# Kernel tuning notes

Hardware: AMD Instinct MI355X
Metric: run time of the kernel (lower is better)

The kernel has to match this reference:

```python
import jax, jax.numpy as jnp
import numpy as np

MARGIN = 0.0625  # init kwarg `margin`; barrier = relu


def setup_inputs() -> dict:
    key = jax.random.key(0)
    k1, k2, k3, k4 = jax.random.split(key, 4)
    B, N, M = 64, 64, 100000
    return {
        "outputs": jax.random.normal(k1, (B, N, 3), dtype=jnp.float32),
        "c2ws": jax.random.normal(k2, (B, 4, 4), dtype=jnp.float32),
        "scene_scales": jax.random.uniform(k3, (B,), dtype=jnp.float32),
        "means": jax.random.normal(k4, (M, 3), dtype=jnp.float32),
    }


def reference(outputs, c2ws, scene_scales, means):
    # aff = R * s (per-batch scaled rotation block), trans = translation column
    aff = c2ws[:, :3, :3] * scene_scales[:, None, None]      # [B,3,3]
    trans = c2ws[:, :3, 3]                                   # [B,3]
    # retrajs = baddbmm(trans, outputs, aff.mT) = outputs @ aff^T + trans
    retrajs = jnp.einsum("bnj,bij->bni", outputs, aff) + trans[:, None, :]
    q = retrajs.reshape(-1, 3)                               # [Q,3], Q = B*N
    # Brute-force nearest neighbor (replaces kd_tree.query); torch_kdtree
    # returns SQUARED euclidean distances, so we keep d^2.
    # d2[q,m] = |q|^2 + |m|^2 - 2 q.m  -> [Q,M] (the dominant memory-bound op)
    d2 = (
        jnp.sum(q * q, axis=-1, keepdims=True)
        + jnp.sum(means * means, axis=-1)[None, :]
        - 2.0 * (q @ means.T)
    )
    dists = jnp.maximum(jnp.min(d2, axis=1), 0.0)            # [Q]
    loss = jnp.mean(jax.nn.relu(-(dists - MARGIN)))
    return loss
```

## Files before the change

### kernel.cpp

```cpp
#include <hip/hip_runtime.h>
#include <hip/hip_bf16.h>

#define MARGIN 0.0625f

#define P 4096
#define M 100000
#define G 500
#define CHUNK 200
#define NPAIR (CHUNK / 2)
#define QS 2
#define R 8
#define HSEG 16

typedef float float2v __attribute__((ext_vector_type(2)));

#define WS_XS_OFF      0
#define WS_YS_OFF      400000
#define WS_ZS_OFF      800000
#define WS_MS_OFF      1200000
#define WS_PARTIAL_OFF 1600000
#define WS_PART2_OFF   9792000

__global__ __launch_bounds__(256) void prep_kernel(
    const float* __restrict__ means,
    float* __restrict__ xs, float* __restrict__ ys,
    float* __restrict__ zs, float* __restrict__ ms,
    float* __restrict__ out)
{
    int idx = blockIdx.x * 256 + threadIdx.x;
    if (idx == 0) out[0] = 0.0f;
    if (idx < M) {
        float x = means[3 * idx + 0];
        float y = means[3 * idx + 1];
        float z = means[3 * idx + 2];
        xs[idx] = -2.0f * x;
        ys[idx] = -2.0f * y;
        zs[idx] = -2.0f * z;
        ms[idx] = fmaf(x, x, fmaf(y, y, z * z));
    }
}

__global__ __launch_bounds__(256, 4) void nn_kernel(
    const float* __restrict__ outputs,
    const float* __restrict__ c2ws,
    const float* __restrict__ scales,
    const float* __restrict__ xs, const float* __restrict__ ys,
    const float* __restrict__ zs, const float* __restrict__ ms,
    float* __restrict__ partial)
{
    const int t  = threadIdx.x;
    const int g  = blockIdx.x;
    const int qs = blockIdx.y;
    const int pbase = qs * (P / QS);
    const int mbase = g * CHUNK;

    __shared__ float2v lxs[NPAIR], lys[NPAIR], lzs[NPAIR], lms[NPAIR];

    if (t < NPAIR) {
        lxs[t] = *(const float2v*)(xs + mbase + 2 * t);
        lys[t] = *(const float2v*)(ys + mbase + 2 * t);
        lzs[t] = *(const float2v*)(zs + mbase + 2 * t);
        lms[t] = *(const float2v*)(ms + mbase + 2 * t);
    }

    float2v qxs[R], qys[R], qzs[R], mn[R];
    float qq[R];
#pragma unroll
    for (int i = 0; i < R; ++i) {
        int p = pbase + i * 256 + t;
        int b = p >> 6;
        float s  = scales[b];
        float o0 = outputs[3 * p + 0];
        float o1 = outputs[3 * p + 1];
        float o2 = outputs[3 * p + 2];
        const float* cw = c2ws + b * 16;
        float q0 = fmaf(s, fmaf(cw[0],  o0, fmaf(cw[1],  o1, cw[2]  * o2)), cw[3]);
        float q1 = fmaf(s, fmaf(cw[4],  o0, fmaf(cw[5],  o1, cw[6]  * o2)), cw[7]);
        float q2 = fmaf(s, fmaf(cw[8],  o0, fmaf(cw[9],  o1, cw[10] * o2)), cw[11]);
        qq[i] = fmaf(q0, q0, fmaf(q1, q1, q2 * q2));
        qxs[i] = (float2v){q0, q0};
        qys[i] = (float2v){q1, q1};
        qzs[i] = (float2v){q2, q2};
        mn[i]  = (float2v){1e30f, 1e30f};
    }

    __syncthreads();

#pragma unroll 4
    for (int j = 0; j < NPAIR; ++j) {
        float2v cx = lxs[j];
        float2v cy = lys[j];
        float2v cz = lzs[j];
        float2v cm = lms[j];
#pragma unroll
        for (int i = 0; i < R; ++i) {
            float2v d = __builtin_elementwise_fma(qzs[i], cz,
                        __builtin_elementwise_fma(qys[i], cy,
                        __builtin_elementwise_fma(qxs[i], cx, cm)));
            mn[i] = __builtin_elementwise_min(mn[i], d);
        }
    }

#pragma unroll
    for (int i = 0; i < R; ++i) {
        int p = pbase + i * 256 + t;
        float m = fminf(mn[i][0], mn[i][1]);
        partial[g * P + p] = fmaxf(qq[i] + m, 0.0f);
    }
}

__global__ __launch_bounds__(256) void reduce1_kernel(
    const float* __restrict__ partial,
    float* __restrict__ partial2)
{
    const int t = threadIdx.x;
    const int s = blockIdx.x;
    const int h = blockIdx.y;
    const int q = s * 256 + t;

    const int gbeg = h * 32;
    const int gend = (gbeg + 32 < G) ? gbeg + 32 : G;

    float m = 1e30f;
#pragma unroll 4
    for (int g = gbeg; g < gend; ++g)
        m = fminf(m, partial[g * P + q]);

    partial2[h * P + q] = m;
}

__global__ __launch_bounds__(256) void reduce2_kernel(
    const float* __restrict__ partial2,
    float* __restrict__ out)
{
    const int t = threadIdx.x;
    const int q = blockIdx.x * 256 + t;

    float m = 1e30f;
#pragma unroll
    for (int h = 0; h < HSEG; ++h)
        m = fminf(m, partial2[h * P + q]);

    float v = fmaxf(MARGIN - m, 0.0f) * (1.0f / (float)P);

#pragma unroll
    for (int off = 32; off > 0; off >>= 1)
        v += __shfl_down(v, off, 64);

    __shared__ float lds[4];
    int wid = t >> 6;
    if ((t & 63) == 0) lds[wid] = v;
    __syncthreads();
    if (t == 0)
        atomicAdd(out, lds[0] + lds[1] + lds[2] + lds[3]);
}

extern "C" void kernel_launch(void* const* d_in, const int* in_sizes, int n_in,
                              void* d_out, int out_size, void* d_ws, size_t ws_size,
                              hipStream_t stream) {
    const float* outputs = (const float*)d_in[0];
    const float* c2ws    = (const float*)d_in[1];
    const float* scales  = (const float*)d_in[2];
    const float* means   = (const float*)d_in[3];

    char* ws = (char*)d_ws;
    float* xs       = (float*)(ws + WS_XS_OFF);
    float* ys       = (float*)(ws + WS_YS_OFF);
    float* zs       = (float*)(ws + WS_ZS_OFF);
    float* ms       = (float*)(ws + WS_MS_OFF);
    float* partial  = (float*)(ws + WS_PARTIAL_OFF);
    float* partial2 = (float*)(ws + WS_PART2_OFF);
    float* out      = (float*)d_out;

    prep_kernel<<<(M + 255) / 256, 256, 0, stream>>>(means, xs, ys, zs, ms, out);
    nn_kernel<<<dim3(G, QS), 256, 0, stream>>>(outputs, c2ws, scales,
                                               xs, ys, zs, ms, partial);
    reduce1_kernel<<<dim3(16, HSEG), 256, 0, stream>>>(partial, partial2);
    reduce2_kernel<<<16, 256, 0, stream>>>(partial2, out);
}
```

Measured before the change: 104.4 us.

## Fuse means prep and partial-min reduction into NN kernel via atomicMin

Removes the separate prep kernel by having each block read raw means, scale them by -2 and compute their squared norms straight into shared memory. The partial-min buffer and two reduction kernels are replaced by a per-query atomicMin on float bits, seeded by a memset to 0xFF, plus a small finish kernel. The inner loop now reads float4 LDS values and splits them into two float2 halves. This removes large global round-trips and launches, at the cost of global atomic contention (500 blocks per query) and strided 3-float means loads in every block.

```diff
diff --git a/kernel.cpp b/kernel.cpp
--- a/kernel.cpp
+++ b/kernel.cpp
@@ -1,5 +1,4 @@
 #include <hip/hip_runtime.h>
-#include <hip/hip_bf16.h>
 
 #define MARGIN 0.0625f
 
@@ -7,46 +6,21 @@
 #define M 100000
 #define G 500
 #define CHUNK 200
-#define NPAIR (CHUNK / 2)
+#define NQUAD (CHUNK / 4)
 #define QS 2
 #define R 8
-#define HSEG 16
 
 typedef float float2v __attribute__((ext_vector_type(2)));
+typedef float float4v __attribute__((ext_vector_type(4)));
 
-#define WS_XS_OFF      0
-#define WS_YS_OFF      400000
-#define WS_ZS_OFF      800000
-#define WS_MS_OFF      1200000
-#define WS_PARTIAL_OFF 1600000
-#define WS_PART2_OFF   9792000
-
-__global__ __launch_bounds__(256) void prep_kernel(
-    const float* __restrict__ means,
-    float* __restrict__ xs, float* __restrict__ ys,
-    float* __restrict__ zs, float* __restrict__ ms,
-    float* __restrict__ out)
-{
-    int idx = blockIdx.x * 256 + threadIdx.x;
-    if (idx == 0) out[0] = 0.0f;
-    if (idx < M) {
-        float x = means[3 * idx + 0];
-        float y = means[3 * idx + 1];
-        float z = means[3 * idx + 2];
-        xs[idx] = -2.0f * x;
-        ys[idx] = -2.0f * y;
-        zs[idx] = -2.0f * z;
-        ms[idx] = fmaf(x, x, fmaf(y, y, z * z));
-    }
-}
+#define WS_PMIN_OFF 0
 
 __global__ __launch_bounds__(256, 4) void nn_kernel(
     const float* __restrict__ outputs,
     const float* __restrict__ c2ws,
     const float* __restrict__ scales,
-    const float* __restrict__ xs, const float* __restrict__ ys,
-    const float* __restrict__ zs, const float* __restrict__ ms,
-    float* __restrict__ partial)
+    const float* __restrict__ means,
+    unsigned int* __restrict__ pmin)
 {
     const int t  = threadIdx.x;
     const int g  = blockIdx.x;
@@ -54,13 +28,15 @@
     const int pbase = qs * (P / QS);
     const int mbase = g * CHUNK;
 
-    __shared__ float2v lxs[NPAIR], lys[NPAIR], lzs[NPAIR], lms[NPAIR];
+    __shared__ float4v lxs[NQUAD], lys[NQUAD], lzs[NQUAD], lms[NQUAD];
 
-    if (t < NPAIR) {
-        lxs[t] = *(const float2v*)(xs + mbase + 2 * t);
-        lys[t] = *(const float2v*)(ys + mbase + 2 * t);
-        lzs[t] = *(const float2v*)(zs + mbase + 2 * t);
-        lms[t] = *(const float2v*)(ms + mbase + 2 * t);
+    if (t < CHUNK) {
+        const float* mp = means + 3 * (mbase + t);
+        float x = mp[0], y = mp[1], z = mp[2];
+        ((float*)lxs)[t] = -2.0f * x;
+        ((float*)lys)[t] = -2.0f * y;
+        ((float*)lzs)[t] = -2.0f * z;
+        ((float*)lms)[t] = fmaf(x, x, fmaf(y, y, z * z));
     }
 
     float2v qxs[R], qys[R], qzs[R], mn[R];
@@ -77,7 +53,7 @@
         float q0 = fmaf(s, fmaf(cw[0],  o0, fmaf(cw[1],  o1, cw[2]  * o2)), cw[3]);
         float q1 = fmaf(s, fmaf(cw[4],  o0, fmaf(cw[5],  o1, cw[6]  * o2)), cw[7]);
         float q2 = fmaf(s, fmaf(cw[8],  o0, fmaf(cw[9],  o1, cw[10] * o2)), cw[11]);
-        qq[i] = fmaf(q0, q0, fmaf(q1, q1, q2 * q2));
+        qq[i]  = fmaf(q0, q0, fmaf(q1, q1, q2 * q2));
         qxs[i] = (float2v){q0, q0};
         qys[i] = (float2v){q1, q1};
         qzs[i] = (float2v){q2, q2};
@@ -86,18 +62,30 @@
 
     __syncthreads();
 
-#pragma unroll 4
-    for (int j = 0; j < NPAIR; ++j) {
-        float2v cx = lxs[j];
-        float2v cy = lys[j];
-        float2v cz = lzs[j];
-        float2v cm = lms[j];
+#pragma unroll 2
+    for (int j = 0; j < NQUAD; ++j) {
+        float4v cx4 = lxs[j];
+        float4v cy4 = lys[j];
+        float4v cz4 = lzs[j];
+        float4v cm4 = lms[j];
+        float2v cx0 = __builtin_shufflevector(cx4, cx4, 0, 1);
+        float2v cx1 = __builtin_shufflevector(cx4, cx4, 2, 3);
+        float2v cy0 = __builtin_shufflevector(cy4, cy4, 0, 1);
+        float2v cy1 = __builtin_shufflevector(cy4, cy4, 2, 3);
+        float2v cz0 = __builtin_shufflevector(cz4, cz4, 0, 1);
+        float2v cz1 = __builtin_shufflevector(cz4, cz4, 2, 3);
+        float2v cm0 = __builtin_shufflevector(cm4, cm4, 0, 1);
+        float2v cm1 = __builtin_shufflevector(cm4, cm4, 2, 3);
 #pragma unroll
         for (int i = 0; i < R; ++i) {
-            float2v d = __builtin_elementwise_fma(qzs[i], cz,
-                        __builtin_elementwise_fma(qys[i], cy,
-                        __builtin_elementwise_fma(qxs[i], cx, cm)));
-            mn[i] = __builtin_elementwise_min(mn[i], d);
+            float2v d0 = __builtin_elementwise_fma(qzs[i], cz0,
+                         __builtin_elementwise_fma(qys[i], cy0,
+                         __builtin_elementwise_fma(qxs[i], cx0, cm0)));
+            float2v d1 = __builtin_elementwise_fma(qzs[i], cz1,
+                         __builtin_elementwise_fma(qys[i], cy1,
+                         __builtin_elementwise_fma(qxs[i], cx1, cm1)));
+            mn[i] = __builtin_elementwise_min(mn[i], d0);
+            mn[i] = __builtin_elementwise_min(mn[i], d1);
         }
     }
 
@@ -105,42 +93,20 @@
     for (int i = 0; i < R; ++i) {
         int p = pbase + i * 256 + t;
         float m = fminf(mn[i][0], mn[i][1]);
-        partial[g * P + p] = fmaxf(qq[i] + m, 0.0f);
+        float d = fmaxf(qq[i] + m, 0.0f);
+        unsigned int bits = __float_as_uint(d);
+        if (bits < pmin[p]) atomicMin(&pmin[p], bits);
     }
 }
 
-__global__ __launch_bounds__(256) void reduce1_kernel(
-    const float* __restrict__ partial,
-    float* __restrict__ partial2)
-{
-    const int t = threadIdx.x;
-    const int s = blockIdx.x;
-    const int h = blockIdx.y;
-    const int q = s * 256 + t;
-
-    const int gbeg = h * 32;
-    const int gend = (gbeg + 32 < G) ? gbeg + 32 : G;
-
-    float m = 1e30f;
-#pragma unroll 4
-    for (int g = gbeg; g < gend; ++g)
-        m = fminf(m, partial[g * P + q]);
-
-    partial2[h * P + q] = m;
-}
-
-__global__ __launch_bounds__(256) void reduce2_kernel(
-    const float* __restrict__ partial2,
+__global__ __launch_bounds__(256) void finish_kernel(
+    const unsigned int* __restrict__ pmin,
     float* __restrict__ out)
 {
     const int t = threadIdx.x;
     const int q = blockIdx.x * 256 + t;
 
-    float m = 1e30f;
-#pragma unroll
-    for (int h = 0; h < HSEG; ++h)
-        m = fminf(m, partial2[h * P + q]);
-
+    float m = __uint_as_float(pmin[q]);
     float v = fmaxf(MARGIN - m, 0.0f) * (1.0f / (float)P);
 
 #pragma unroll
@@ -163,18 +129,12 @@
     const float* scales  = (const float*)d_in[2];
     const float* means   = (const float*)d_in[3];
 
-    char* ws = (char*)d_ws;
-    float* xs       = (float*)(ws + WS_XS_OFF);
-    float* ys       = (float*)(ws + WS_YS_OFF);
-    float* zs       = (float*)(ws + WS_ZS_OFF);
-    float* ms       = (float*)(ws + WS_MS_OFF);
-    float* partial  = (float*)(ws + WS_PARTIAL_OFF);
-    float* partial2 = (float*)(ws + WS_PART2_OFF);
-    float* out      = (float*)d_out;
+    unsigned int* pmin = (unsigned int*)((char*)d_ws + WS_PMIN_OFF);
+    float* out = (float*)d_out;
 
-    prep_kernel<<<(M + 255) / 256, 256, 0, stream>>>(means, xs, ys, zs, ms, out);
-    nn_kernel<<<dim3(G, QS), 256, 0, stream>>>(outputs, c2ws, scales,
-                                               xs, ys, zs, ms, partial);
-    reduce1_kernel<<<dim3(16, HSEG), 256, 0, stream>>>(partial, partial2);
-    reduce2_kernel<<<16, 256, 0, stream>>>(partial2, out);
+    hipMemsetAsync(pmin, 0xFF, P * sizeof(unsigned int), stream);
+    hipMemsetAsync(out, 0, sizeof(float), stream);
+
+    nn_kernel<<<dim3(G, QS), 256, 0, stream>>>(outputs, c2ws, scales, means, pmin);
+    finish_kernel<<<P / 256, 256, 0, stream>>>(pmin, out);
 }
```

Result: slower. 124.0 us (+18.7%).
